# Kernel tuning notes

Hardware: AMD Instinct MI355X
Metric: run time of the kernel (lower is better)

Reference implementation:

```python
import jax, jax.numpy as jnp
import numpy as np

DIM = 256
CDIM = 512
HEADS = 8
DIM_HEAD = 32
HID = HEADS * DIM_HEAD          # 256
MLP_DIM = int(DIM * 2.5)        # 640
B, T, TC = 8, 8192, 8192
GROUPS = 32
EPS = 1e-5


def setup_inputs() -> dict:
    key = jax.random.key(0)
    ks = jax.random.split(key, 12)
    w = lambda k, shape: jax.random.normal(k, shape, jnp.float32) * 0.02
    return {
        "x": jax.random.normal(ks[0], (B, DIM, T), jnp.float32),
        "c": jax.random.normal(ks[1], (B, CDIM, TC), jnp.float32),
        # self-attn (LinearAttention)
        "W_qkv": w(ks[2], (3 * HID, DIM)),
        "W_so": w(ks[3], (DIM, HID)), "b_so": jnp.zeros((DIM,), jnp.float32),
        "sa_g": jnp.ones((DIM,), jnp.float32), "sa_b": jnp.zeros((DIM,), jnp.float32),
        # cross-attn (LinearAttentionC)
        "W_cq": w(ks[4], (HID, DIM)),
        "W_ckv": w(ks[5], (2 * HID, CDIM)),
        "W_co": w(ks[6], (DIM, HID)), "b_co": jnp.zeros((DIM,), jnp.float32),
        "ca_g": jnp.ones((DIM,), jnp.float32), "ca_b": jnp.zeros((DIM,), jnp.float32),
        # MLP
        "W_m1": w(ks[7], (MLP_DIM, DIM)), "b_m1": jnp.zeros((MLP_DIM,), jnp.float32),
        "W_m2": w(ks[8], (DIM, MLP_DIM)), "b_m2": jnp.zeros((DIM,), jnp.float32),
        # pre-norms
        "nm_g": jnp.ones((DIM,), jnp.float32), "nm_b": jnp.zeros((DIM,), jnp.float32),
        "nm1_g": jnp.ones((DIM,), jnp.float32), "nm1_b": jnp.zeros((DIM,), jnp.float32),
        "nm2_g": jnp.ones((DIM,), jnp.float32), "nm2_b": jnp.zeros((DIM,), jnp.float32),
        "nm3_g": jnp.ones((CDIM,), jnp.float32), "nm3_b": jnp.zeros((CDIM,), jnp.float32),
    }


def group_norm(x, g, b):
    Bx, C, Tx = x.shape
    xg = x.reshape(Bx, GROUPS, C // GROUPS, Tx)
    mu = xg.mean(axis=(2, 3), keepdims=True)
    var = ((xg - mu) ** 2).mean(axis=(2, 3), keepdims=True)
    xn = ((xg - mu) * jax.lax.rsqrt(var + EPS)).reshape(Bx, C, Tx)
    return xn * g[None, :, None] + b[None, :, None]


def conv1(x, W, b=None):
    # 1x1 Conv1d == channel matmul: W [out, in], x [b, in, t]
    y = jnp.einsum('oc,bct->bot', W, x)
    return y if b is None else y + b[None, :, None]


def split_heads(t):
    Bx, HC, Tx = t.shape
    return t.reshape(Bx, HEADS, HC // HEADS, Tx)  # b h c t


def linear_attention(q, k, v):
    # q,k,v: [b, h, d, t]
    scale = DIM_HEAD ** -0.5
    q = jax.nn.softmax(q, axis=-2) * scale   # softmax over feature dim d
    k = jax.nn.softmax(k, axis=-1)           # softmax over time t
    ctx = jnp.einsum('bhdn,bhen->bhde', k, v)   # [b,h,d,e] tiny per-head context
    out = jnp.einsum('bhde,bhdn->bhen', ctx, q)
    Bx, H, E, Tx = out.shape
    return out.reshape(Bx, H * E, Tx)  # b (h c) t


def reference(x, c, W_qkv, W_so, b_so, sa_g, sa_b,
              W_cq, W_ckv, W_co, b_co, ca_g, ca_b,
              W_m1, b_m1, W_m2, b_m2,
              nm_g, nm_b, nm1_g, nm1_b, nm2_g, nm2_b, nm3_g, nm3_b):
    # --- self linear attention + residual ---
    h = group_norm(x, nm_g, nm_b)
    q, k, v = map(split_heads, jnp.split(conv1(h, W_qkv), 3, axis=1))
    o = linear_attention(q, k, v)
    o = group_norm(conv1(o, W_so, b_so), sa_g, sa_b)
    x = o + x
    # --- cross linear attention + residual ---
    h = group_norm(x, nm1_g, nm1_b)
    cn = group_norm(c, nm3_g, nm3_b)
    q = split_heads(conv1(h, W_cq))
    k, v = map(split_heads, jnp.split(conv1(cn, W_ckv), 2, axis=1))
    o = linear_attention(q, k, v)
    o = group_norm(conv1(o, W_co, b_co), ca_g, ca_b)
    x = o + x
    # --- SiLU MLP + residual ---
    h = group_norm(x, nm2_g, nm2_b)
    h = jax.nn.silu(conv1(h, W_m1, b_m1))
    x = conv1(h, W_m2, b_m2) + x
    return x
```

## Files before the change

### kernel.cpp

```cpp
#include <hip/hip_runtime.h>
#include <cmath>

typedef unsigned short u16;
typedef __attribute__((ext_vector_type(8))) __bf16 bf16x8;
typedef __attribute__((ext_vector_type(4))) float f32x4;

#define DEV static __device__ __forceinline__

DEV float b2f(u16 u){ union{unsigned i; float f;} v; v.i=((unsigned)u)<<16; return v.f; }
DEV u16 f2b(float f){ union{float f; unsigned i;} v; v.f=f; unsigned r = v.i + 0x7FFFu + ((v.i>>16)&1u); return (u16)(r>>16); }

#define GLL(g,l) __builtin_amdgcn_global_load_lds((const __attribute__((address_space(1))) void*)(g), (__attribute__((address_space(3))) void*)(l), 16, 0, 0)

__global__ void k_zero(float* p, int n){ int i = blockIdx.x*256+threadIdx.x; if(i<n) p[i]=0.f; }

__global__ void k_cvtall(const float* __restrict__ s0,const float* __restrict__ s1,
                         const float* __restrict__ s2,const float* __restrict__ s3,
                         const float* __restrict__ s4,const float* __restrict__ s5,
                         const float* __restrict__ s6, u16* __restrict__ d){
  int i = blockIdx.x*256 + threadIdx.x;
  if (i >= 983040) return;
  const float* s; int off;
  if      (i < 196608){ s=s0; off=0; }
  else if (i < 262144){ s=s1; off=196608; }
  else if (i < 327680){ s=s2; off=262144; }
  else if (i < 589824){ s=s3; off=327680; }
  else if (i < 655360){ s=s4; off=589824; }
  else if (i < 819200){ s=s5; off=655360; }
  else                { s=s6; off=819200; }
  d[i] = f2b(s[i-off]);
}

__global__ void k_stats2(const float* __restrict__ x, const float* __restrict__ c,
                         float* __restrict__ statx, float* __restrict__ statc){
  const int blk = blockIdx.x;
  const float* src; float* stat; long base; int chunk;
  if (blk < 2048){ chunk = blk>>3; base = (long)chunk*65536 + (long)(blk&7)*8192; src=x; stat=statx; }
  else { const int b2 = blk-2048; chunk = b2>>4; base = (long)chunk*131072 + (long)(b2&15)*8192; src=c; stat=statc; }
  const float4* xp = (const float4*)(src+base);
  float s=0.f, s2=0.f;
  #pragma unroll
  for (int i=0;i<8;i++){
    float4 v = xp[i*256 + threadIdx.x];
    s  += v.x+v.y+v.z+v.w;
    s2 += v.x*v.x+v.y*v.y+v.z*v.z+v.w*v.w;
  }
  __shared__ float a[256], a2[256];
  a[threadIdx.x]=s; a2[threadIdx.x]=s2;
  __syncthreads();
  for (int off=128; off>0; off>>=1){
    if (threadIdx.x < off){ a[threadIdx.x]+=a[threadIdx.x+off]; a2[threadIdx.x]+=a2[threadIdx.x+off]; }
    __syncthreads();
  }
  if (threadIdx.x==0){
    atomicAdd(&stat[chunk*2],   a[0]);
    atomicAdd(&stat[chunk*2+1], a2[0]);
  }
}

template<bool WRAW>
__global__ void k_trans(const float* __restrict__ src, u16* __restrict__ dstRaw,
                        u16* __restrict__ dstB, const float* __restrict__ stat,
                        const float* __restrict__ gw, const float* __restrict__ bw,
                        int C, int chsh, float inv_n){
  const int b = blockIdx.z;
  const int t0 = blockIdx.x*64, c0 = blockIdx.y*64;
  __shared__ float tile[64][65];
  #pragma unroll
  for (int p=0;p<4;p++){
    const int cc = (threadIdx.x>>4) + p*16, tt = (threadIdx.x&15)*4;
    const float4 v = *(const float4*)&src[((long)b*C + c0+cc)*8192 + t0+tt];
    tile[cc][tt+0]=v.x; tile[cc][tt+1]=v.y; tile[cc][tt+2]=v.z; tile[cc][tt+3]=v.w;
  }
  __syncthreads();
  #pragma unroll
  for (int p=0;p<4;p++){
    const int tt = (threadIdx.x>>4) + p*16, c4 = (threadIdx.x&15)*4;
    u16 nbi[4], rbi[4];
    #pragma unroll
    for (int j=0;j<4;j++){
      const float raw = tile[c4+j][tt];
      const int ch = c0+c4+j, gr = ch>>chsh;
      const float s = stat[(b*32+gr)*2], s2 = stat[(b*32+gr)*2+1];
      const float mu = s*inv_n;
      const float rs = rsqrtf(s2*inv_n - mu*mu + 1e-5f);
      nbi[j] = f2b((raw-mu)*rs*gw[ch]+bw[ch]);
      rbi[j] = f2b(raw);
    }
    const long db = ((long)b*8192 + t0+tt)*C + c0+c4;
    ushort4 nb; nb.x=nbi[0]; nb.y=nbi[1]; nb.z=nbi[2]; nb.w=nbi[3];
    *(ushort4*)&dstB[db] = nb;
    if (WRAW){ ushort4 rv; rv.x=rbi[0]; rv.y=rbi[1]; rv.z=rbi[2]; rv.w=rbi[3]; *(ushort4*)&dstRaw[db] = rv; }
  }
}

template<bool OUTB, bool BIAS, bool SILU, bool RES, bool STATS, bool SPLIT>
__global__ __launch_bounds__(256,2) void k_gemm(
    const u16* __restrict__ A, const u16* __restrict__ W,
    float* __restrict__ outF, u16* __restrict__ outB,
    const float* __restrict__ bias, const u16* __restrict__ res,
    float* __restrict__ stat, int K, int O)
{
  __shared__ u16 As[128*64];
  __shared__ u16 Ws[128*64];
  __shared__ float sb[128][2];
  const int tid = threadIdx.x;
  const int wv = tid>>6, lane = tid&63;
  const long t0 = (long)blockIdx.y*128;
  const int o0 = blockIdx.x*128;
  const int wt = (wv>>1)*64, wo = (wv&1)*64;
  const int lr = lane>>3, lc = (lane&7)*8;
  f32x4 acc[4][4] = {};
  for (int kc = 0; kc < K; kc += 64){
    #pragma unroll
    for (int it = 0; it < 4; ++it){
      const int r = wv*32 + it*8;
      GLL(A + (t0 + r + lr)*(long)K + kc + lc, &As[r*64]);
      GLL(W + (long)(o0 + r + lr)*K + kc + lc, &Ws[r*64]);
    }
    __syncthreads();
    #pragma unroll
    for (int ks=0; ks<2; ++ks){
      const int kb = ks*32 + (lane>>4)*8;
      bf16x8 af[4], bfr[4];
      #pragma unroll
      for (int i=0;i<4;i++) af[i]  = *(const bf16x8*)&As[(wt + i*16 + (lane&15))*64 + kb];
      #pragma unroll
      for (int j=0;j<4;j++) bfr[j] = *(const bf16x8*)&Ws[(wo + j*16 + (lane&15))*64 + kb];
      #pragma unroll
      for (int i=0;i<4;i++)
        #pragma unroll
        for (int j=0;j<4;j++)
          acc[i][j] = __builtin_amdgcn_mfma_f32_16x16x32_bf16(af[i], bfr[j], acc[i][j], 0, 0, 0);
    }
    __syncthreads();
  }
  if (STATS){
    if (tid < 128){ sb[tid][0]=0.f; sb[tid][1]=0.f; }
    __syncthreads();
  }
  const int q = lane>>4, cc = lane&15;
  #pragma unroll
  for (int j=0;j<4;j++){
    const int o = o0 + wo + j*16 + cc;
    const float bv = BIAS ? bias[o] : 0.f;
    float ts=0.f, ts2=0.f;
    #pragma unroll
    for (int i=0;i<4;i++){
      const long tb = t0 + wt + i*16 + q*4;
      #pragma unroll
      for (int r=0;r<4;r++){
        float v = acc[i][j][r] + bv;
        if (SILU) v = v * (1.f/(1.f + __expf(-v)));
        long idx;
        if (SPLIT) idx = ((long)(o>>8)<<24) + (tb + r)*256 + (o&255);
        else       idx = (tb + r)*(long)O + o;
        if (RES) v += b2f(res[idx]);
        if (STATS){ ts += v; ts2 += v*v; }
        if (OUTB) outB[idx] = f2b(v); else outF[idx] = v;
      }
    }
    if (STATS){
      const int ol = wo + j*16 + cc;
      atomicAdd(&sb[ol][0], ts);
      atomicAdd(&sb[ol][1], ts2);
    }
  }
  if (STATS){
    __syncthreads();
    if (tid < 16){
      float u=0.f, u2=0.f;
      #pragma unroll
      for (int j2=0;j2<8;j2++){ u += sb[tid*8+j2][0]; u2 += sb[tid*8+j2][1]; }
      const int bb = (int)(t0>>13);
      atomicAdd(&stat[(bb*32 + (o0>>3) + tid)*2],   u);
      atomicAdd(&stat[(bb*32 + (o0>>3) + tid)*2+1], u2);
    }
  }
}

__global__ __launch_bounds__(256,2) void k_ctx(const u16* __restrict__ kp, const u16* __restrict__ vp,
                                               float* __restrict__ part){
  const int tid = threadIdx.x;
  const int b = blockIdx.x >> 6, seg = blockIdx.x & 63;
  const int h = tid>>5, d = tid&31;
  __shared__ u16 kb[16][256];
  __shared__ float vf[16][260];
  float acc[32];
  #pragma unroll
  for (int e=0;e<32;e++) acc[e]=0.f;
  float ks = 0.f;
  const long rb = (long)b*8192 + seg*128;
  const int w = tid>>6, sub = tid&63;
  for (int tc=0; tc<128; tc+=16){
    #pragma unroll
    for (int p=0;p<4;p++){
      const int row = p*4 + w;
      const long rowbase = (rb + tc + row)*256;
      if (sub < 32){
        uint4 val = *(const uint4*)(kp + rowbase + sub*8);
        *(uint4*)&kb[row][sub*8] = val;
      } else {
        const int s2 = sub-32;
        uint4 val = *(const uint4*)(vp + rowbase + s2*8);
        const u16* vs = (const u16*)&val;
        float4 f0 = {b2f(vs[0]),b2f(vs[1]),b2f(vs[2]),b2f(vs[3])};
        float4 f1 = {b2f(vs[4]),b2f(vs[5]),b2f(vs[6]),b2f(vs[7])};
        *(float4*)&vf[row][s2*8] = f0;
        *(float4*)&vf[row][s2*8+4] = f1;
      }
    }
    __syncthreads();
    #pragma unroll
    for (int r=0;r<16;r++){
      const float kpv = __expf(b2f(kb[r][h*32+d]));
      ks += kpv;
      #pragma unroll
      for (int e4=0;e4<8;e4++){
        const float4 v4 = *(const float4*)&vf[r][h*32+e4*4];
        acc[e4*4+0] += kpv*v4.x; acc[e4*4+1] += kpv*v4.y;
        acc[e4*4+2] += kpv*v4.z; acc[e4*4+3] += kpv*v4.w;
      }
    }
    __syncthreads();
  }
  float* pb = part + (long)blockIdx.x*8448;
  #pragma unroll
  for (int e=0;e<32;e++) pb[e*256 + tid] = acc[e];
  pb[8192 + tid] = ks;
}

__global__ void k_ctxred(const float* __restrict__ part, float* __restrict__ ctx,
                         float* __restrict__ ksumF){
  if (blockIdx.x >= 256){
    const int j = (blockIdx.x-256)*256 + threadIdx.x;
    #pragma unroll
    for (int q=0;q<4;q++){
      const int idx = j*4+q;
      const int b = idx>>8, cch = idx&255;
      float s=0.f;
      for (int g=0; g<64; g++) s += part[((long)(b*64+g))*8448 + 8192 + cch];
      ksumF[idx] = s;
    }
    return;
  }
  const int i = blockIdx.x*256 + threadIdx.x;
  const int b = i>>13, r = i&8191;
  float s=0.f;
  for (int g=0; g<64; g++) s += part[((long)(b*64+g))*8448 + r];
  ctx[i] = s;
}

__global__ void k_attnout(const u16* __restrict__ q, const float* __restrict__ ctx,
                          const float* __restrict__ ksumF, u16* __restrict__ out){
  const int b = blockIdx.x >> 8, t0 = (blockIdx.x & 255)*32;
  __shared__ float cs[8512];
  for (int i=threadIdx.x; i<8192; i+=256){
    const int e=i>>8, cch=i&255;
    cs[(cch>>5)*1064 + (cch&31)*33 + e] = ctx[(b<<13) + i] / ksumF[b*256 + cch];
  }
  __syncthreads();
  const int t = t0 + (threadIdx.x>>3), h = threadIdx.x&7;
  const u16* qp = q + ((long)b*8192 + t)*256 + h*32;
  uint4 qv[4];
  #pragma unroll
  for (int j=0;j<4;j++) qv[j] = ((const uint4*)qp)[j];
  const u16* qs = (const u16*)qv;
  float qe[32]; float ssum = 0.f;
  #pragma unroll
  for (int dd=0; dd<32; dd++){ qe[dd] = __expf(b2f(qs[dd])); ssum += qe[dd]; }
  const float inv = 0.17677669529663687f / ssum;
  float o[32];
  #pragma unroll
  for (int e=0;e<32;e++) o[e]=0.f;
  const float* ch = &cs[h*1064];
  #pragma unroll
  for (int dd=0; dd<32; dd++){
    const float w = qe[dd]*inv;
    #pragma unroll
    for (int e=0;e<32;e++) o[e] += w * ch[dd*33+e];
  }
  u16 ob[32];
  #pragma unroll
  for (int e=0;e<32;e++) ob[e] = f2b(o[e]);
  uint4* op = (uint4*)(out + ((long)b*8192 + t)*256 + h*32);
  const uint4* obv = (const uint4*)ob;
  #pragma unroll
  for (int j=0;j<4;j++) op[j] = obv[j];
}

__global__ void k_gnres(const u16* __restrict__ conv, u16* __restrict__ xr,
                        const float* __restrict__ sums_in, float* __restrict__ sums_out,
                        const float* __restrict__ g, const float* __restrict__ bt){
  const int blk = blockIdx.x;
  const int b = blk>>7;
  const long base = (long)blk*4096;
  const int tid = threadIdx.x;
  const int c0 = (tid<<2)&255;
  const int gr = c0>>3;
  const float s = sums_in[(b*32+gr)*2], s2 = sums_in[(b*32+gr)*2+1];
  const float mu = s*(1.f/65536.f);
  const float rs = rsqrtf(s2*(1.f/65536.f) - mu*mu + 1e-5f);
  float gg[4], bb[4];
  #pragma unroll
  for (int j=0;j<4;j++){ gg[j] = g[c0+j]*rs; bb[j] = bt[c0+j] - mu*gg[j]; }
  float ts=0.f, ts2=0.f;
  for (int it=0; it<16; ++it){
    const long i4 = base + it*256 + tid;
    ushort4 cv = ((const ushort4*)conv)[i4];
    ushort4 rv = ((const ushort4*)xr)[i4];
    float ov[4];
    const float ci[4] = {b2f(cv.x),b2f(cv.y),b2f(cv.z),b2f(cv.w)};
    const float ri[4] = {b2f(rv.x),b2f(rv.y),b2f(rv.z),b2f(rv.w)};
    #pragma unroll
    for (int j=0;j<4;j++){
      ov[j] = ci[j]*gg[j] + bb[j] + ri[j];
      ts += ov[j]; ts2 += ov[j]*ov[j];
    }
    ushort4 o4; o4.x=f2b(ov[0]); o4.y=f2b(ov[1]); o4.z=f2b(ov[2]); o4.w=f2b(ov[3]);
    ((ushort4*)xr)[i4] = o4;
  }
  __shared__ float grp[32][2];
  if (tid<32){ grp[tid][0]=0.f; grp[tid][1]=0.f; }
  __syncthreads();
  atomicAdd(&grp[gr][0], ts);
  atomicAdd(&grp[gr][1], ts2);
  __syncthreads();
  if (tid<32){
    atomicAdd(&sums_out[(b*32+tid)*2],   grp[tid][0]);
    atomicAdd(&sums_out[(b*32+tid)*2+1], grp[tid][1]);
  }
}

__global__ void k_gnapply(const u16* __restrict__ x, u16* __restrict__ o,
                          const float* __restrict__ sums, const float* __restrict__ g,
                          const float* __restrict__ bt){
  const long i4 = (long)blockIdx.x*256 + threadIdx.x;
  const int b = (int)(i4 >> 19);
  const int c0 = (int)((i4<<2) & 255);
  ushort4 v = ((const ushort4*)x)[i4];
  const float vi[4] = {b2f(v.x),b2f(v.y),b2f(v.z),b2f(v.w)};
  u16 obi[4];
  #pragma unroll
  for (int j=0;j<4;j++){
    const int ch = c0+j, gr=ch>>3;
    const float s = sums[(b*32+gr)*2], s2 = sums[(b*32+gr)*2+1];
    const float mu = s*(1.f/65536.f);
    const float rs = rsqrtf(s2*(1.f/65536.f)-mu*mu+1e-5f);
    obi[j] = f2b((vi[j]-mu)*rs*g[ch]+bt[ch]);
  }
  ushort4 ob; ob.x=obi[0]; ob.y=obi[1]; ob.z=obi[2]; ob.w=obi[3];
  ((ushort4*)o)[i4] = ob;
}

__global__ void k_final(const float* __restrict__ y, float* __restrict__ out){
  const int b = blockIdx.z;
  const int t0 = blockIdx.x*64, c0 = blockIdx.y*64;
  __shared__ float tile[64][65];
  #pragma unroll
  for (int p=0;p<4;p++){
    const int tt = (threadIdx.x>>4) + p*16, c4 = (threadIdx.x&15)*4;
    const float4 v = *(const float4*)&y[((long)b*8192 + t0+tt)*256 + c0+c4];
    tile[c4+0][tt]=v.x; tile[c4+1][tt]=v.y; tile[c4+2][tt]=v.z; tile[c4+3][tt]=v.w;
  }
  __syncthreads();
  #pragma unroll
  for (int p=0;p<4;p++){
    const int cc = (threadIdx.x>>4) + p*16, t4 = (threadIdx.x&15)*4;
    float4 v = {tile[cc][t4], tile[cc][t4+1], tile[cc][t4+2], tile[cc][t4+3]};
    *(float4*)&out[((long)b*256 + c0+cc)*8192 + t0+t4] = v;
  }
}

extern "C" void kernel_launch(void* const* d_in, const int* in_sizes, int n_in,
                              void* d_out, int out_size, void* d_ws, size_t ws_size,
                              hipStream_t stream){
  (void)in_sizes; (void)n_in; (void)out_size; (void)ws_size;
  const float* x   = (const float*)d_in[0];
  const float* c   = (const float*)d_in[1];
  const float* W_qkv=(const float*)d_in[2];
  const float* W_so =(const float*)d_in[3];
  const float* b_so =(const float*)d_in[4];
  const float* sa_g =(const float*)d_in[5];
  const float* sa_b =(const float*)d_in[6];
  const float* W_cq =(const float*)d_in[7];
  const float* W_ckv=(const float*)d_in[8];
  const float* W_co =(const float*)d_in[9];
  const float* b_co =(const float*)d_in[10];
  const float* ca_g =(const float*)d_in[11];
  const float* ca_b =(const float*)d_in[12];
  const float* W_m1 =(const float*)d_in[13];
  const float* b_m1 =(const float*)d_in[14];
  const float* W_m2 =(const float*)d_in[15];
  const float* b_m2 =(const float*)d_in[16];
  const float* nm_g =(const float*)d_in[17];
  const float* nm_b =(const float*)d_in[18];
  const float* nm1_g=(const float*)d_in[19];
  const float* nm1_b=(const float*)d_in[20];
  const float* nm2_g=(const float*)d_in[21];
  const float* nm2_b=(const float*)d_in[22];
  const float* nm3_g=(const float*)d_in[23];
  const float* nm3_b=(const float*)d_in[24];
  float* out = (float*)d_out;

  char* ws = (char*)d_ws;
  const size_t MB = 1024ull*1024ull;
  u16* wbf  = (u16*)ws;
  u16* wQKV = wbf;
  u16* wSO  = wbf + 196608;
  u16* wCQ  = wbf + 262144;
  u16* wCKV = wbf + 327680;
  u16* wCO  = wbf + 589824;
  u16* wM1  = wbf + 655360;
  u16* wM2  = wbf + 819200;
  float* stats = (float*)(ws + 2*MB);
  float* xstat = stats;
  float* cstat = stats + 512;
  float* so_sum= stats + 1024;
  float* x1_sum= stats + 1536;
  float* co_sum= stats + 2048;
  float* x2_sum= stats + 2560;
  float* ksumF = stats + 3072;
  float* ctxb  = stats + 8192;
  u16*   xT    = (u16*)(ws + 4*MB);
  u16*   hbf   = (u16*)(ws + 68*MB);
  float* part  = (float*)(ws + 68*MB);
  u16*   cnbf  = (u16*)(ws + 100*MB);
  u16*   qkvb  = (u16*)(ws + 164*MB);
  u16*   kvb   = (u16*)(ws + 264*MB);
  u16*   convb = (u16*)(ws + 264*MB);
  float* convF = (float*)(ws + 264*MB);
  u16*   attno = (u16*)(ws + 328*MB);
  const long SEG = 1L<<24;

  k_zero<<<12,256,0,stream>>>(stats, 3072);
  k_cvtall<<<3840,256,0,stream>>>(W_qkv, W_so, W_cq, W_ckv, W_co, W_m1, W_m2, wbf);

  k_stats2<<<6144,256,0,stream>>>(x, c, xstat, cstat);
  k_trans<true ><<<dim3(128,4,8),256,0,stream>>>(x, xT, hbf, xstat, nm_g, nm_b, 256, 3, 1.f/65536.f);
  k_trans<false><<<dim3(128,8,8),256,0,stream>>>(c, nullptr, cnbf, cstat, nm3_g, nm3_b, 512, 4, 1.f/131072.f);
  k_gemm<true,false,false,false,false,true><<<dim3(6,512),256,0,stream>>>(hbf, wQKV, nullptr, qkvb, nullptr, nullptr, nullptr, 256, 768);
  k_ctx<<<512,256,0,stream>>>(qkvb+SEG, qkvb+2*SEG, part);
  k_ctxred<<<258,256,0,stream>>>(part, ctxb, ksumF);
  k_attnout<<<2048,256,0,stream>>>(qkvb, ctxb, ksumF, attno);
  k_gemm<true,true,false,false,true,false><<<dim3(2,512),256,0,stream>>>(attno, wSO, nullptr, convb, b_so, nullptr, so_sum, 256, 256);
  k_gnres<<<1024,256,0,stream>>>(convb, xT, so_sum, x1_sum, sa_g, sa_b);

  k_gnapply<<<16384,256,0,stream>>>(xT, hbf, x1_sum, nm1_g, nm1_b);
  k_gemm<true,false,false,false,false,false><<<dim3(2,512),256,0,stream>>>(hbf, wCQ, nullptr, qkvb, nullptr, nullptr, nullptr, 256, 256);
  k_gemm<true,false,false,false,false,true><<<dim3(4,512),256,0,stream>>>(cnbf, wCKV, nullptr, kvb, nullptr, nullptr, nullptr, 512, 512);
  k_ctx<<<512,256,0,stream>>>(kvb, kvb+SEG, part);
  k_ctxred<<<258,256,0,stream>>>(part, ctxb, ksumF);
  k_attnout<<<2048,256,0,stream>>>(qkvb, ctxb, ksumF, attno);
  k_gemm<true,true,false,false,true,false><<<dim3(2,512),256,0,stream>>>(attno, wCO, nullptr, convb, b_co, nullptr, co_sum, 256, 256);
  k_gnres<<<1024,256,0,stream>>>(convb, xT, co_sum, x2_sum, ca_g, ca_b);

  k_gnapply<<<16384,256,0,stream>>>(xT, hbf, x2_sum, nm2_g, nm2_b);
  k_gemm<true,true,true,false,false,false><<<dim3(5,512),256,0,stream>>>(hbf, wM1, nullptr, qkvb, b_m1, nullptr, nullptr, 256, 640);
  k_gemm<false,true,false,true,false,false><<<dim3(2,512),256,0,stream>>>(qkvb, wM2, convF, nullptr, b_m2, xT, nullptr, 640, 256);
  k_final<<<dim3(128,4,8),256,0,stream>>>(convF, out);
}
```

Before: 974.6 us.

## Fold GroupNorm affine into per-batch GEMM weights and bias, fuse stats into transpose

Each pre-norm GroupNorm feeding a 1x1 conv is now folded algebraically into a per-batch scaled bf16 weight matrix and bias (k_fold), so the GEMMs read the raw transposed activations directly. This removes the k_gnapply passes and the normalized-copy writes for x and c. The separate stats pass is fused into the transpose kernel, which accumulates group sums while tiling. In exchange it adds per-batch weight materialisation and a weight pointer offset in the GEMM. Folding normalization into bf16 weights changes rounding, and the variance is computed from raw sums.

```diff
diff --git a/kernel.cpp b/kernel.cpp
--- a/kernel.cpp
+++ b/kernel.cpp
@@ -14,83 +14,83 @@
 
 __global__ void k_zero(float* p, int n){ int i = blockIdx.x*256+threadIdx.x; if(i<n) p[i]=0.f; }
 
-__global__ void k_cvtall(const float* __restrict__ s0,const float* __restrict__ s1,
-                         const float* __restrict__ s2,const float* __restrict__ s3,
-                         const float* __restrict__ s4,const float* __restrict__ s5,
-                         const float* __restrict__ s6, u16* __restrict__ d){
+__global__ void k_cvt3(const float* __restrict__ s0,const float* __restrict__ s1,
+                       const float* __restrict__ s2, u16* __restrict__ d){
   int i = blockIdx.x*256 + threadIdx.x;
-  if (i >= 983040) return;
+  if (i >= 294912) return;
   const float* s; int off;
-  if      (i < 196608){ s=s0; off=0; }
-  else if (i < 262144){ s=s1; off=196608; }
-  else if (i < 327680){ s=s2; off=262144; }
-  else if (i < 589824){ s=s3; off=327680; }
-  else if (i < 655360){ s=s4; off=589824; }
-  else if (i < 819200){ s=s5; off=655360; }
-  else                { s=s6; off=819200; }
+  if      (i < 65536){ s=s0; off=0; }
+  else if (i < 131072){ s=s1; off=65536; }
+  else                { s=s2; off=131072; }
   d[i] = f2b(s[i-off]);
 }
 
-__global__ void k_stats2(const float* __restrict__ x, const float* __restrict__ c,
-                         float* __restrict__ statx, float* __restrict__ statc){
-  const int blk = blockIdx.x;
-  const float* src; float* stat; long base; int chunk;
-  if (blk < 2048){ chunk = blk>>3; base = (long)chunk*65536 + (long)(blk&7)*8192; src=x; stat=statx; }
-  else { const int b2 = blk-2048; chunk = b2>>4; base = (long)chunk*131072 + (long)(b2&15)*8192; src=c; stat=statc; }
-  const float4* xp = (const float4*)(src+base);
-  float s=0.f, s2=0.f;
-  #pragma unroll
-  for (int i=0;i<8;i++){
-    float4 v = xp[i*256 + threadIdx.x];
-    s  += v.x+v.y+v.z+v.w;
-    s2 += v.x*v.x+v.y*v.y+v.z*v.z+v.w*v.w;
-  }
-  __shared__ float a[256], a2[256];
-  a[threadIdx.x]=s; a2[threadIdx.x]=s2;
-  __syncthreads();
-  for (int off=128; off>0; off>>=1){
-    if (threadIdx.x < off){ a[threadIdx.x]+=a[threadIdx.x+off]; a2[threadIdx.x]+=a2[threadIdx.x+off]; }
-    __syncthreads();
-  }
-  if (threadIdx.x==0){
-    atomicAdd(&stat[chunk*2],   a[0]);
-    atomicAdd(&stat[chunk*2+1], a2[0]);
-  }
-}
-
-template<bool WRAW>
-__global__ void k_trans(const float* __restrict__ src, u16* __restrict__ dstRaw,
-                        u16* __restrict__ dstB, const float* __restrict__ stat,
-                        const float* __restrict__ gw, const float* __restrict__ bw,
-                        int C, int chsh, float inv_n){
+__global__ void k_fold(const float* __restrict__ W, const float* __restrict__ g,
+                       const float* __restrict__ beta, const float* __restrict__ base,
+                       const float* __restrict__ stats, u16* __restrict__ Wb,
+                       float* __restrict__ biasb, int O, int K, int chsh, float inv_n){
+  const int o = blockIdx.x, b = blockIdx.y;
+  const int tid = threadIdx.x;
+  float bp = 0.f;
+  for (int k = tid; k < K; k += 256){
+    const int gr = k >> chsh;
+    const float s = stats[(b*32+gr)*2], s2 = stats[(b*32+gr)*2+1];
+    const float mu = s*inv_n;
+    const float rs = rsqrtf(s2*inv_n - mu*mu + 1e-5f);
+    const float w = W[(long)o*K + k];
+    const float gg = g[k]*rs;
+    Wb[((long)b*O + o)*K + k] = f2b(w*gg);
+    bp += w*(beta[k] - mu*gg);
+  }
+  __shared__ float red[256];
+  red[tid] = bp; __syncthreads();
+  for (int off=128; off>0; off>>=1){ if (tid<off) red[tid]+=red[tid+off]; __syncthreads(); }
+  if (tid==0) biasb[b*O+o] = red[0] + (base ? base[o] : 0.f);
+}
+
+template<int CHSH>
+__global__ void k_transs(const float* __restrict__ src, u16* __restrict__ dstRaw,
+                         float* __restrict__ stat, int C){
   const int b = blockIdx.z;
   const int t0 = blockIdx.x*64, c0 = blockIdx.y*64;
+  const int tid = threadIdx.x;
   __shared__ float tile[64][65];
+  __shared__ float grp[16];
+  if (tid < 16) grp[tid] = 0.f;
+  float s_acc[4], s2_acc[4];
   #pragma unroll
   for (int p=0;p<4;p++){
-    const int cc = (threadIdx.x>>4) + p*16, tt = (threadIdx.x&15)*4;
+    const int cc = (tid>>4) + p*16, tt = (tid&15)*4;
     const float4 v = *(const float4*)&src[((long)b*C + c0+cc)*8192 + t0+tt];
     tile[cc][tt+0]=v.x; tile[cc][tt+1]=v.y; tile[cc][tt+2]=v.z; tile[cc][tt+3]=v.w;
+    s_acc[p]  = v.x+v.y+v.z+v.w;
+    s2_acc[p] = v.x*v.x+v.y*v.y+v.z*v.z+v.w*v.w;
   }
   __syncthreads();
   #pragma unroll
   for (int p=0;p<4;p++){
-    const int tt = (threadIdx.x>>4) + p*16, c4 = (threadIdx.x&15)*4;
-    u16 nbi[4], rbi[4];
-    #pragma unroll
-    for (int j=0;j<4;j++){
-      const float raw = tile[c4+j][tt];
-      const int ch = c0+c4+j, gr = ch>>chsh;
-      const float s = stat[(b*32+gr)*2], s2 = stat[(b*32+gr)*2+1];
-      const float mu = s*inv_n;
-      const float rs = rsqrtf(s2*inv_n - mu*mu + 1e-5f);
-      nbi[j] = f2b((raw-mu)*rs*gw[ch]+bw[ch]);
-      rbi[j] = f2b(raw);
-    }
-    const long db = ((long)b*8192 + t0+tt)*C + c0+c4;
-    ushort4 nb; nb.x=nbi[0]; nb.y=nbi[1]; nb.z=nbi[2]; nb.w=nbi[3];
-    *(ushort4*)&dstB[db] = nb;
-    if (WRAW){ ushort4 rv; rv.x=rbi[0]; rv.y=rbi[1]; rv.z=rbi[2]; rv.w=rbi[3]; *(ushort4*)&dstRaw[db] = rv; }
+    float s = s_acc[p], s2 = s2_acc[p];
+    #pragma unroll
+    for (int m=1; m<16; m<<=1){ s += __shfl_xor(s, m); s2 += __shfl_xor(s2, m); }
+    if ((tid&15)==0){
+      const int gl = ((tid>>4) + p*16) >> CHSH;
+      atomicAdd(&grp[gl*2],   s);
+      atomicAdd(&grp[gl*2+1], s2);
+    }
+  }
+  #pragma unroll
+  for (int p=0;p<4;p++){
+    const int tt = (tid>>4) + p*16, c4 = (tid&15)*4;
+    u16 rbi[4];
+    #pragma unroll
+    for (int j=0;j<4;j++) rbi[j] = f2b(tile[c4+j][tt]);
+    ushort4 rv; rv.x=rbi[0]; rv.y=rbi[1]; rv.z=rbi[2]; rv.w=rbi[3];
+    *(ushort4*)&dstRaw[((long)b*8192 + t0+tt)*C + c0+c4] = rv;
+  }
+  __syncthreads();
+  const int ngr = 64>>CHSH;
+  if (tid < ngr*2){
+    atomicAdd(&stat[((b*32) + (c0>>CHSH))*2 + tid], grp[tid]);
   }
 }
 
@@ -99,7 +99,7 @@
     const u16* __restrict__ A, const u16* __restrict__ W,
     float* __restrict__ outF, u16* __restrict__ outB,
     const float* __restrict__ bias, const u16* __restrict__ res,
-    float* __restrict__ stat, int K, int O)
+    float* __restrict__ stat, int K, int O, long wsb, int bsb)
 {
   __shared__ u16 As[128*64];
   __shared__ u16 Ws[128*64];
@@ -108,6 +108,8 @@
   const int wv = tid>>6, lane = tid&63;
   const long t0 = (long)blockIdx.y*128;
   const int o0 = blockIdx.x*128;
+  const int bb = (int)(t0>>13);
+  const u16* Wp = W + (long)bb*wsb;
   const int wt = (wv>>1)*64, wo = (wv&1)*64;
   const int lr = lane>>3, lc = (lane&7)*8;
   f32x4 acc[4][4] = {};
@@ -116,7 +118,7 @@
     for (int it = 0; it < 4; ++it){
       const int r = wv*32 + it*8;
       GLL(A + (t0 + r + lr)*(long)K + kc + lc, &As[r*64]);
-      GLL(W + (long)(o0 + r + lr)*K + kc + lc, &Ws[r*64]);
+      GLL(Wp + (long)(o0 + r + lr)*K + kc + lc, &Ws[r*64]);
     }
     __syncthreads();
     #pragma unroll
@@ -143,7 +145,7 @@
   #pragma unroll
   for (int j=0;j<4;j++){
     const int o = o0 + wo + j*16 + cc;
-    const float bv = BIAS ? bias[o] : 0.f;
+    const float bv = BIAS ? bias[bsb*bb + o] : 0.f;
     float ts=0.f, ts2=0.f;
     #pragma unroll
     for (int i=0;i<4;i++){
@@ -172,7 +174,6 @@
       float u=0.f, u2=0.f;
       #pragma unroll
       for (int j2=0;j2<8;j2++){ u += sb[tid*8+j2][0]; u2 += sb[tid*8+j2][1]; }
-      const int bb = (int)(t0>>13);
       atomicAdd(&stat[(bb*32 + (o0>>3) + tid)*2],   u);
       atomicAdd(&stat[(bb*32 + (o0>>3) + tid)*2+1], u2);
     }
@@ -330,27 +331,6 @@
     atomicAdd(&sums_out[(b*32+tid)*2],   grp[tid][0]);
     atomicAdd(&sums_out[(b*32+tid)*2+1], grp[tid][1]);
   }
-}
-
-__global__ void k_gnapply(const u16* __restrict__ x, u16* __restrict__ o,
-                          const float* __restrict__ sums, const float* __restrict__ g,
-                          const float* __restrict__ bt){
-  const long i4 = (long)blockIdx.x*256 + threadIdx.x;
-  const int b = (int)(i4 >> 19);
-  const int c0 = (int)((i4<<2) & 255);
-  ushort4 v = ((const ushort4*)x)[i4];
-  const float vi[4] = {b2f(v.x),b2f(v.y),b2f(v.z),b2f(v.w)};
-  u16 obi[4];
-  #pragma unroll
-  for (int j=0;j<4;j++){
-    const int ch = c0+j, gr=ch>>3;
-    const float s = sums[(b*32+gr)*2], s2 = sums[(b*32+gr)*2+1];
-    const float mu = s*(1.f/65536.f);
-    const float rs = rsqrtf(s2*(1.f/65536.f)-mu*mu+1e-5f);
-    obi[j] = f2b((vi[j]-mu)*rs*g[ch]+bt[ch]);
-  }
-  ushort4 ob; ob.x=obi[0]; ob.y=obi[1]; ob.z=obi[2]; ob.w=obi[3];
-  ((ushort4*)o)[i4] = ob;
 }
 
 __global__ void k_final(const float* __restrict__ y, float* __restrict__ out){
@@ -405,15 +385,10 @@
 
   char* ws = (char*)d_ws;
   const size_t MB = 1024ull*1024ull;
-  u16* wbf  = (u16*)ws;
-  u16* wQKV = wbf;
-  u16* wSO  = wbf + 196608;
-  u16* wCQ  = wbf + 262144;
-  u16* wCKV = wbf + 327680;
-  u16* wCO  = wbf + 589824;
-  u16* wM1  = wbf + 655360;
-  u16* wM2  = wbf + 819200;
-  float* stats = (float*)(ws + 2*MB);
+  u16* wSO = (u16*)ws;
+  u16* wCO = wSO + 65536;
+  u16* wM2 = wCO + 65536;
+  float* stats = (float*)(ws + 1*MB);
   float* xstat = stats;
   float* cstat = stats + 512;
   float* so_sum= stats + 1024;
@@ -422,41 +397,50 @@
   float* x2_sum= stats + 2560;
   float* ksumF = stats + 3072;
   float* ctxb  = stats + 8192;
-  u16*   xT    = (u16*)(ws + 4*MB);
-  u16*   hbf   = (u16*)(ws + 68*MB);
-  float* part  = (float*)(ws + 68*MB);
-  u16*   cnbf  = (u16*)(ws + 100*MB);
-  u16*   qkvb  = (u16*)(ws + 164*MB);
-  u16*   kvb   = (u16*)(ws + 264*MB);
-  u16*   convb = (u16*)(ws + 264*MB);
-  float* convF = (float*)(ws + 264*MB);
-  u16*   attno = (u16*)(ws + 328*MB);
+  float* bQKV = (float*)(ws + 2*MB);
+  float* bCKV = bQKV + 6144;
+  float* bCQ  = bCKV + 4096;
+  float* bM1  = bCQ + 2048;
+  u16* wQKVb = (u16*)(ws + 3*MB);
+  u16* wCKVb = (u16*)(ws + 6*MB);
+  u16* wCQb  = (u16*)(ws + 10*MB);
+  u16* wM1b  = (u16*)(ws + 11*MB);
+  u16*   xT    = (u16*)(ws + 16*MB);
+  u16*   cT    = (u16*)(ws + 48*MB);
+  float* part  = (float*)(ws + 112*MB);
+  u16*   qkvb  = (u16*)(ws + 136*MB);
+  u16*   kvb   = (u16*)(ws + 232*MB);
+  u16*   convb = kvb;
+  float* convF = (float*)kvb;
+  u16*   attno = (u16*)(ws + 296*MB);
   const long SEG = 1L<<24;
 
   k_zero<<<12,256,0,stream>>>(stats, 3072);
-  k_cvtall<<<3840,256,0,stream>>>(W_qkv, W_so, W_cq, W_ckv, W_co, W_m1, W_m2, wbf);
-
-  k_stats2<<<6144,256,0,stream>>>(x, c, xstat, cstat);
-  k_trans<true ><<<dim3(128,4,8),256,0,stream>>>(x, xT, hbf, xstat, nm_g, nm_b, 256, 3, 1.f/65536.f);
-  k_trans<false><<<dim3(128,8,8),256,0,stream>>>(c, nullptr, cnbf, cstat, nm3_g, nm3_b, 512, 4, 1.f/131072.f);
-  k_gemm<true,false,false,false,false,true><<<dim3(6,512),256,0,stream>>>(hbf, wQKV, nullptr, qkvb, nullptr, nullptr, nullptr, 256, 768);
+  k_cvt3<<<1152,256,0,stream>>>(W_so, W_co, W_m2, wSO);
+
+  k_transs<3><<<dim3(128,4,8),256,0,stream>>>(x, xT, xstat, 256);
+  k_transs<4><<<dim3(128,8,8),256,0,stream>>>(c, cT, cstat, 512);
+
+  k_fold<<<dim3(768,8),256,0,stream>>>(W_qkv, nm_g, nm_b, nullptr, xstat, wQKVb, bQKV, 768, 256, 3, 1.f/65536.f);
+  k_fold<<<dim3(512,8),256,0,stream>>>(W_ckv, nm3_g, nm3_b, nullptr, cstat, wCKVb, bCKV, 512, 512, 4, 1.f/131072.f);
+  k_gemm<true,true,false,false,false,true><<<dim3(6,512),256,0,stream>>>(xT, wQKVb, nullptr, qkvb, bQKV, nullptr, nullptr, 256, 768, 196608, 768);
   k_ctx<<<512,256,0,stream>>>(qkvb+SEG, qkvb+2*SEG, part);
   k_ctxred<<<258,256,0,stream>>>(part, ctxb, ksumF);
   k_attnout<<<2048,256,0,stream>>>(qkvb, ctxb, ksumF, attno);
-  k_gemm<true,true,false,false,true,false><<<dim3(2,512),256,0,stream>>>(attno, wSO, nullptr, convb, b_so, nullptr, so_sum, 256, 256);
+  k_gemm<true,true,false,false,true,false><<<dim3(2,512),256,0,stream>>>(attno, wSO, nullptr, convb, b_so, nullptr, so_sum, 256, 256, 0, 0);
   k_gnres<<<1024,256,0,stream>>>(convb, xT, so_sum, x1_sum, sa_g, sa_b);
 
-  k_gnapply<<<16384,256,0,stream>>>(xT, hbf, x1_sum, nm1_g, nm1_b);
-  k_gemm<true,false,false,false,false,false><<<dim3(2,512),256,0,stream>>>(hbf, wCQ, nullptr, qkvb, nullptr, nullptr, nullptr, 256, 256);
-  k_gemm<true,false,false,false,false,true><<<dim3(4,512),256,0,stream>>>(cnbf, wCKV, nullptr, kvb, nullptr, nullptr, nullptr, 512, 512);
+  k_fold<<<dim3(256,8),256,0,stream>>>(W_cq, nm1_g, nm1_b, nullptr, x1_sum, wCQb, bCQ, 256, 256, 3, 1.f/65536.f);
+  k_gemm<true,true,false,false,false,false><<<dim3(2,512),256,0,stream>>>(xT, wCQb, nullptr, qkvb, bCQ, nullptr, nullptr, 256, 256, 65536, 256);
+  k_gemm<true,true,false,false,false,true><<<dim3(4,512),256,0,stream>>>(cT, wCKVb, nullptr, kvb, bCKV, nullptr, nullptr, 512, 512, 262144, 512);
   k_ctx<<<512,256,0,stream>>>(kvb, kvb+SEG, part);
   k_ctxred<<<258,256,0,stream>>>(part, ctxb, ksumF);
   k_attnout<<<2048,256,0,stream>>>(qkvb, ctxb, ksumF, attno);
-  k_gemm<true,true,false,false,true,false><<<dim3(2,512),256,0,stream>>>(attno, wCO, nullptr, convb, b_co, nullptr, co_sum, 256, 256);
+  k_gemm<true,true,false,false,true,false><<<dim3(2,512),256,0,stream>>>(attno, wCO, nullptr, convb, b_co, nullptr, co_sum, 256, 256, 0, 0);
   k_gnres<<<1024,256,0,stream>>>(convb, xT, co_sum, x2_sum, ca_g, ca_b);
 
-  k_gnapply<<<16384,256,0,stream>>>(xT, hbf, x2_sum, nm2_g, nm2_b);
-  k_gemm<true,true,true,false,false,false><<<dim3(5,512),256,0,stream>>>(hbf, wM1, nullptr, qkvb, b_m1, nullptr, nullptr, 256, 640);
-  k_gemm<false,true,false,true,false,false><<<dim3(2,512),256,0,stream>>>(qkvb, wM2, convF, nullptr, b_m2, xT, nullptr, 640, 256);
+  k_fold<<<dim3(640,8),256,0,stream>>>(W_m1, nm2_g, nm2_b, b_m1, x2_sum, wM1b, bM1, 640, 256, 3, 1.f/65536.f);
+  k_gemm<true,true,true,false,false,false><<<dim3(5,512),256,0,stream>>>(xT, wM1b, nullptr, qkvb, bM1, nullptr, nullptr, 256, 640, 163840, 640);
+  k_gemm<false,true,false,true,false,false><<<dim3(2,512),256,0,stream>>>(qkvb, wM2, convF, nullptr, b_m2, xT, nullptr, 640, 256, 0, 0);
   k_final<<<dim3(128,4,8),256,0,stream>>>(convF, out);
 }
```

Result: faster. 934.8 us (-4.1%).
